# Performance work log

Hardware: AMD Instinct MI355X
Metric: run time of the kernel (lower is better)

The kernel has to match this reference:

```python
import jax, jax.numpy as jnp
import numpy as np


def setup_inputs() -> dict:
    key = jax.random.key(0)
    k_in, k_w = jax.random.split(key)
    input = jax.random.normal(k_in, (16, 64, 64, 512), dtype=jnp.float32)
    weight = jax.random.normal(k_w, (512, 512), dtype=jnp.float32)
    return {"input": input, "weight": weight}


def reference(input, weight):
    # Faithful to the torch source, including its quirky (weight*weight).sum(0)
    # (sum over the vocab axis -> (embed_dim,) vector, broadcast over vocab
    # columns; valid here because vocab_size == embed_dim).
    batch_dims, embed_dim = input.shape[:-1], input.shape[-1]
    x = input.reshape(-1, embed_dim)                     # (N, D)
    dists = -2.0 * jnp.einsum("nd,vd->nv", x, weight) + jnp.sum(weight * weight, axis=0)[None, :]
    idxes = jnp.argmin(dists, axis=1)                    # (N,)
    values = weight[idxes].reshape(*batch_dims, embed_dim)
    return values
```

## Files before the change

### kernel.cpp

```cpp
#include <hip/hip_runtime.h>


#define DIM   512
#define VOCAB 512
#define EPS_GAP 0.18f
#define RBATCH 8

typedef float f32x4 __attribute__((ext_vector_type(4)));
typedef _Float16 f16x8 __attribute__((ext_vector_type(8)));
typedef unsigned long long u64;

__device__ inline u64 packkey(float s, int v){
    unsigned u = __float_as_uint(s);
    u = (u & 0x80000000u) ? ~u : (u | 0x80000000u);
    return (((u64)u) << 32) | (unsigned)(~v);
}
__device__ inline float keyscore(u64 k){
    unsigned e = (unsigned)(k >> 32);
    return __uint_as_float((e & 0x80000000u) ? (e & 0x7fffffffu) : ~e);
}
__device__ inline int keyv(u64 k){ return (int)(~(unsigned)(k & 0xffffffffu)); }
__device__ inline u64 umax64(u64 a, u64 b){ return a > b ? a : b; }
__device__ inline u64 umin64(u64 a, u64 b){ return a < b ? a : b; }

__global__ void colsumsq_kernel(const float* __restrict__ w, float* __restrict__ c){
    const int v = blockIdx.x;
    const int lane = threadIdx.x;
    double s = 0.0;
    for (int i = lane; i < DIM; i += 64){
        const float wv = w[i * VOCAB + v];
        s += (double)wv * (double)wv;
    }
    #pragma unroll
    for (int m = 1; m <= 32; m <<= 1) s += __shfl_xor(s, m, 64);
    if (lane == 0) c[v] = (float)s;
}

__global__ void prep_w(const float* __restrict__ w,
                       _Float16* __restrict__ whc,
                       unsigned* __restrict__ cnt){
    const int i = blockIdx.x * 256 + threadIdx.x;
    const int v = i >> 9, k = i & 511;
    const int d = (k >> 5) * 16384 + ((k >> 3) & 3) * 4096 + v * 8 + (k & 7);
    whc[d] = (_Float16)w[i];
    if (i == 0) *cnt = 0u;
}

__launch_bounds__(256, 4)
__global__ void k1_scores(const float* __restrict__ x,
                          const _Float16* __restrict__ whc,
                          const float* __restrict__ cg,
                          const float* __restrict__ w,
                          float* __restrict__ out,
                          int* __restrict__ list,
                          unsigned* __restrict__ cnt){
    __shared__ __align__(16) _Float16 Ah[16384];
    __shared__ u64 mergeK[32][4][2];
    __shared__ int idx_s[32];

    const int t = threadIdx.x;
    const int lane = t & 63, wv = t >> 6, quad = lane >> 4, lm = lane & 15;
    const int cb = wv << 7;
    const long rbase = (long)blockIdx.x * 32;
    const float* xblk = x + rbase * DIM;

    f32x4 acc[2][8];
    #pragma unroll
    for (int ct = 0; ct < 8; ++ct){
        const float bias = -0.5f * cg[cb + ct * 16 + lm];
        f32x4 z; z[0] = bias; z[1] = bias; z[2] = bias; z[3] = bias;
        acc[0][ct] = z; acc[1][ct] = z;
    }

    #pragma unroll 4
    for (int jj = 0; jj < 16; ++jj){
        const int j   = jj * 256 + t;
        const int row = (j >> 3) & 31;
        const int k4  = (j & 7) | ((j >> 8) << 3);
        const int kk  = k4 << 2;
        const float4 a4 = *(const float4*)(xblk + (long)row * DIM + kk);
        union { _Float16 h[4]; ushort4 u; } cv;
        cv.h[0] = (_Float16)a4.x;
        cv.h[1] = (_Float16)a4.y;
        cv.h[2] = (_Float16)a4.z;
        cv.h[3] = (_Float16)a4.w;
        const int d = (((kk >> 5) * 4 + ((kk >> 3) & 3)) * 32 + row) * 8 + (kk & 7);
        *(ushort4*)&Ah[d] = cv.u;
    }
    __syncthreads();

    for (int ch = 0; ch < 16; ++ch){
        f16x8 ah0 = *(const f16x8*)&Ah[((ch * 4 + quad) * 32 + lm) * 8];
        f16x8 ah1 = *(const f16x8*)&Ah[((ch * 4 + quad) * 32 + 16 + lm) * 8];
        const _Float16* bb = whc + ch * 16384 + quad * 4096;
        #pragma unroll
        for (int ct = 0; ct < 8; ++ct){
            const f16x8 bh = *(const f16x8*)(bb + (cb + ct * 16 + lm) * 8);
            acc[0][ct] = __builtin_amdgcn_mfma_f32_16x16x32_f16(ah0, bh, acc[0][ct], 0, 0, 0);
            acc[1][ct] = __builtin_amdgcn_mfma_f32_16x16x32_f16(ah1, bh, acc[1][ct], 0, 0, 0);
        }
    }

    #pragma unroll
    for (int rt = 0; rt < 2; ++rt){
        #pragma unroll
        for (int reg = 0; reg < 4; ++reg){
            u64 b1 = 0, b2 = 0;
            #pragma unroll
            for (int ct = 0; ct < 8; ++ct){
                const u64 key = packkey(acc[rt][ct][reg], cb + ct * 16 + lm);
                if (key > b1){ b2 = b1; b1 = key; }
                else if (key > b2){ b2 = key; }
            }
            #pragma unroll
            for (int m = 1; m <= 8; m <<= 1){
                const u64 o1 = __shfl_xor(b1, m, 64);
                const u64 o2 = __shfl_xor(b2, m, 64);
                const u64 n1 = umax64(b1, o1);
                b2 = umax64(umin64(b1, o1), umax64(b2, o2));
                b1 = n1;
            }
            if (lm == 0){
                const int row = rt * 16 + quad * 4 + reg;
                mergeK[row][wv][0] = b1;
                mergeK[row][wv][1] = b2;
            }
        }
    }
    __syncthreads();
    if (t < 32){
        u64 p1 = mergeK[t][0][0], p2 = mergeK[t][0][1];
        #pragma unroll
        for (int i = 1; i < 4; ++i){
            const u64 q1 = mergeK[t][i][0], q2 = mergeK[t][i][1];
            const u64 n1 = umax64(p1, q1);
            p2 = umax64(umin64(p1, q1), umax64(p2, q2));
            p1 = n1;
        }
        idx_s[t] = keyv(p1);
        if (keyscore(p1) - keyscore(p2) < EPS_GAP){
            const unsigned p = atomicAdd(cnt, 1u);
            list[p] = (int)(rbase + t);
        }
    }
    __syncthreads();

    for (int rr = 0; rr < 32; rr += 2){
        const int row  = rr + (t >> 7);
        const int col  = (t & 127) << 2;
        const int vidx = idx_s[row];
        const float4 val = *(const float4*)(w + (long)vidx * DIM + col);
        *(float4*)(out + (rbase + row) * DIM + col) = val;
    }
}

__global__ void refine_rows(const float* __restrict__ x, const float* __restrict__ w,
                            const float* __restrict__ cg, const int* __restrict__ list,
                            const unsigned* __restrict__ cnt, float* __restrict__ out){
    __shared__ __align__(16) float xs[RBATCH][DIM];
    __shared__ u64 wk[RBATCH][4];
    __shared__ int bestv_s[RBATCH];
    const int t = threadIdx.x;
    const int lane = t & 63, wvq = t >> 6;
    const int n = (int)*cnt;
    for (int base = blockIdx.x * RBATCH; base < n; base += gridDim.x * RBATCH){
        const int m = (n - base < RBATCH) ? (n - base) : RBATCH;
        __syncthreads();
        for (int s = t; s < m * 128; s += 256){
            const int r = s >> 7, c = (s & 127) << 2;
            *(float4*)&xs[r][c] = *(const float4*)(x + (long)list[base + r] * DIM + c);
        }
        __syncthreads();
        u64 best[RBATCH];
        #pragma unroll
        for (int r = 0; r < RBATCH; ++r) best[r] = 0;
        #pragma unroll
        for (int vv = 0; vv < 2; ++vv){
            const int v = t + vv * 256;
            const float* wr = w + (long)v * DIM;
            float s[RBATCH];
            #pragma unroll
            for (int r = 0; r < RBATCH; ++r) s[r] = -0.5f * cg[v];
            for (int k = 0; k < DIM; k += 4){
                const float4 w4 = *(const float4*)(wr + k);
                #pragma unroll
                for (int r = 0; r < RBATCH; ++r){
                    const float4 x4 = *(const float4*)&xs[r][k];
                    s[r] = fmaf(w4.x, x4.x, s[r]);
                    s[r] = fmaf(w4.y, x4.y, s[r]);
                    s[r] = fmaf(w4.z, x4.z, s[r]);
                    s[r] = fmaf(w4.w, x4.w, s[r]);
                }
            }
            #pragma unroll
            for (int r = 0; r < RBATCH; ++r)
                best[r] = umax64(best[r], packkey(s[r], v));
        }
        #pragma unroll
        for (int r = 0; r < RBATCH; ++r){
            u64 b = best[r];
            #pragma unroll
            for (int mm = 1; mm <= 32; mm <<= 1) b = umax64(b, __shfl_xor(b, mm, 64));
            if (lane == 0) wk[r][wvq] = b;
        }
        __syncthreads();
        if (t < RBATCH){
            const u64 b = umax64(umax64(wk[t][0], wk[t][1]), umax64(wk[t][2], wk[t][3]));
            bestv_s[t] = keyv(b);
        }
        __syncthreads();
        for (int s = t; s < m * 128; s += 256){
            const int r = s >> 7, c = (s & 127) << 2;
            *(float4*)(out + (long)list[base + r] * DIM + c) =
                *(const float4*)(w + (long)bestv_s[r] * DIM + c);
        }
    }
}

__launch_bounds__(256)
__global__ void fallback_full(const float* __restrict__ x, const float* __restrict__ w,
                              float* __restrict__ out){
    __shared__ __align__(16) float As[16][68];
    __shared__ __align__(16) float Bs[16][VOCAB];
    __shared__ int   idx_sf[64];
    __shared__ float c_s[VOCAB];

    const int t  = threadIdx.x;
    const int tx = t & 31;
    const int ty = t >> 5;
    const long rbase = (long)blockIdx.x * 64;
    const float* xblk = x + rbase * DIM;

    for (int vv = t; vv < VOCAB; vv += 256){
        double s = 0.0;
        for (int i = 0; i < DIM; ++i){
            const float wvv = w[i * VOCAB + vv];
            s += (double)wvv * (double)wvv;
        }
        c_s[vv] = (float)s;
    }

    float acc[8][16];
    #pragma unroll
    for (int r = 0; r < 8; ++r)
        #pragma unroll
        for (int j = 0; j < 16; ++j) acc[r][j] = 0.0f;

    for (int k0 = 0; k0 < DIM; k0 += 16){
        __syncthreads();
        {
            const int r  = t >> 2;
            const int kq = (t & 3) << 2;
            const float4 a4 = *(const float4*)(xblk + (long)r * DIM + k0 + kq);
            As[kq + 0][r] = a4.x; As[kq + 1][r] = a4.y;
            As[kq + 2][r] = a4.z; As[kq + 3][r] = a4.w;
        }
        #pragma unroll
        for (int vb = 0; vb < 8; ++vb){
            const int v  = (t >> 2) + (vb << 6);
            const int kq = (t & 3) << 2;
            const float4 b4 = *(const float4*)(w + (long)v * DIM + k0 + kq);
            Bs[kq + 0][v] = b4.x; Bs[kq + 1][v] = b4.y;
            Bs[kq + 2][v] = b4.z; Bs[kq + 3][v] = b4.w;
        }
        __syncthreads();

        #pragma unroll
        for (int k = 0; k < 16; ++k){
            float a[8];
            const float4 a03 = *(const float4*)&As[k][ty * 8];
            const float4 a47 = *(const float4*)&As[k][ty * 8 + 4];
            a[0] = a03.x; a[1] = a03.y; a[2] = a03.z; a[3] = a03.w;
            a[4] = a47.x; a[5] = a47.y; a[6] = a47.z; a[7] = a47.w;
            float b[16];
            #pragma unroll
            for (int j = 0; j < 16; ++j) b[j] = Bs[k][tx + (j << 5)];
            #pragma unroll
            for (int r = 0; r < 8; ++r)
                #pragma unroll
                for (int j = 0; j < 16; ++j)
                    acc[r][j] = fmaf(a[r], b[j], acc[r][j]);
        }
    }

    #pragma unroll
    for (int r = 0; r < 8; ++r){
        float best = acc[r][0] - 0.5f * c_s[tx];
        int   bv   = tx;
        #pragma unroll
        for (int j = 1; j < 16; ++j){
            const float s = acc[r][j] - 0.5f * c_s[tx + (j << 5)];
            if (s > best){ best = s; bv = tx + (j << 5); }
        }
        unsigned u = __float_as_uint(best);
        u = (u & 0x80000000u) ? ~u : (u | 0x80000000u);
        u64 key = ((u64)u << 32) | (unsigned)(~(unsigned)bv);
        #pragma unroll
        for (int m = 1; m <= 16; m <<= 1){
            const u64 o = __shfl_xor(key, m, 64);
            if (o > key) key = o;
        }
        if (tx == 0) idx_sf[ty * 8 + r] = (int)(~(unsigned)(key & 0xFFFFFFFFull));
    }
    __syncthreads();

    for (int rr = 0; rr < 64; rr += 2){
        const int row  = rr + (t >> 7);
        const int col  = (t & 127) << 2;
        const int vidx = idx_sf[row];
        const float4 val = *(const float4*)(w + (long)vidx * DIM + col);
        *(float4*)(out + (rbase + row) * DIM + col) = val;
    }
}

extern "C" void kernel_launch(void* const* d_in, const int* in_sizes, int n_in,
                              void* d_out, int out_size, void* d_ws, size_t ws_size,
                              hipStream_t stream){
    const float* x = (const float*)d_in[0];
    const float* w = (const float*)d_in[1];
    float* out = (float*)d_out;
    const int rows = in_sizes[0] / DIM;

    const size_t whc_off  = 0;
    const size_t c_off    = whc_off + (size_t)DIM * VOCAB * 2;
    const size_t list_off = c_off   + (size_t)VOCAB * 4;
    const size_t cnt_off  = list_off + (size_t)rows * 4;
    const size_t need     = cnt_off + 16;

    if (ws_size >= need){
        _Float16* whc  = (_Float16*)((char*)d_ws + whc_off);
        float*    c    = (float*)((char*)d_ws + c_off);
        int*      list = (int*)((char*)d_ws + list_off);
        unsigned* cnt  = (unsigned*)((char*)d_ws + cnt_off);

        prep_w<<<(DIM * VOCAB) / 256, 256, 0, stream>>>(w, whc, cnt);
        colsumsq_kernel<<<VOCAB, 64, 0, stream>>>(w, c);
        k1_scores<<<rows / 32, 256, 0, stream>>>(x, whc, c, w, out, list, cnt);
        refine_rows<<<512, 256, 0, stream>>>(x, w, c, list, cnt, out);
    } else {
        fallback_full<<<rows / 64, 256, 0, stream>>>(x, w, out);
    }
}
```

Measured before the change: 331.0 us.

## Fuse weight prep with column norms and split gather into separate kernel

Replaces the separate fp16 weight-conversion and column-sum-of-squares kernels with one coalesced kernel that accumulates norms via double atomics into a memset-cleared buffer. Moves the output gather out of the scoring kernel into a dedicated kernel driven by a per-row index array in workspace. Also raises the unroll of the input-staging loop. This adds a memset and an extra launch plus index round-trip through global memory, but frees the scoring kernel from the gather tail and removes the strided column-sum reads.

```diff
diff --git a/kernel.cpp b/kernel.cpp
--- a/kernel.cpp
+++ b/kernel.cpp
@@ -23,40 +23,38 @@
 __device__ inline u64 umax64(u64 a, u64 b){ return a > b ? a : b; }
 __device__ inline u64 umin64(u64 a, u64 b){ return a < b ? a : b; }
 
-__global__ void colsumsq_kernel(const float* __restrict__ w, float* __restrict__ c){
-    const int v = blockIdx.x;
-    const int lane = threadIdx.x;
-    double s = 0.0;
-    for (int i = lane; i < DIM; i += 64){
-        const float wv = w[i * VOCAB + v];
-        s += (double)wv * (double)wv;
-    }
-    #pragma unroll
-    for (int m = 1; m <= 32; m <<= 1) s += __shfl_xor(s, m, 64);
-    if (lane == 0) c[v] = (float)s;
-}
-
-__global__ void prep_w(const float* __restrict__ w,
-                       _Float16* __restrict__ whc,
-                       unsigned* __restrict__ cnt){
-    const int i = blockIdx.x * 256 + threadIdx.x;
-    const int v = i >> 9, k = i & 511;
-    const int d = (k >> 5) * 16384 + ((k >> 3) & 3) * 4096 + v * 8 + (k & 7);
-    whc[d] = (_Float16)w[i];
-    if (i == 0) *cnt = 0u;
+__global__ void prep_fused(const float* __restrict__ w,
+                           _Float16* __restrict__ whc,
+                           double* __restrict__ cgd){
+    const int t  = threadIdx.x;
+    const int r0 = blockIdx.x * 4;
+    const int c0 = t * 2;
+    double s0 = 0.0, s1 = 0.0;
+    #pragma unroll
+    for (int rr = 0; rr < 4; ++rr){
+        const int row = r0 + rr;
+        const float2 v = *(const float2*)(w + (long)row * VOCAB + c0);
+        s0 += (double)v.x * (double)v.x;
+        s1 += (double)v.y * (double)v.y;
+        union { _Float16 h[2]; unsigned u; } cv;
+        cv.h[0] = (_Float16)v.x;
+        cv.h[1] = (_Float16)v.y;
+        const int d = ((c0 >> 5) * 16384) + (((c0 >> 3) & 3) * 4096) + row * 8 + (c0 & 7);
+        *(unsigned*)&whc[d] = cv.u;
+    }
+    atomicAdd(&cgd[c0],     s0);
+    atomicAdd(&cgd[c0 + 1], s1);
 }
 
 __launch_bounds__(256, 4)
 __global__ void k1_scores(const float* __restrict__ x,
                           const _Float16* __restrict__ whc,
-                          const float* __restrict__ cg,
-                          const float* __restrict__ w,
-                          float* __restrict__ out,
+                          const double* __restrict__ cgd,
+                          int* __restrict__ idx,
                           int* __restrict__ list,
                           unsigned* __restrict__ cnt){
     __shared__ __align__(16) _Float16 Ah[16384];
     __shared__ u64 mergeK[32][4][2];
-    __shared__ int idx_s[32];
 
     const int t = threadIdx.x;
     const int lane = t & 63, wv = t >> 6, quad = lane >> 4, lm = lane & 15;
@@ -67,12 +65,12 @@
     f32x4 acc[2][8];
     #pragma unroll
     for (int ct = 0; ct < 8; ++ct){
-        const float bias = -0.5f * cg[cb + ct * 16 + lm];
+        const float bias = -0.5f * (float)cgd[cb + ct * 16 + lm];
         f32x4 z; z[0] = bias; z[1] = bias; z[2] = bias; z[3] = bias;
         acc[0][ct] = z; acc[1][ct] = z;
     }
 
-    #pragma unroll 4
+    #pragma unroll 8
     for (int jj = 0; jj < 16; ++jj){
         const int j   = jj * 256 + t;
         const int row = (j >> 3) & 31;
@@ -137,25 +135,31 @@
             p2 = umax64(umin64(p1, q1), umax64(p2, q2));
             p1 = n1;
         }
-        idx_s[t] = keyv(p1);
+        idx[rbase + t] = keyv(p1);
         if (keyscore(p1) - keyscore(p2) < EPS_GAP){
             const unsigned p = atomicAdd(cnt, 1u);
             list[p] = (int)(rbase + t);
         }
     }
-    __syncthreads();
-
-    for (int rr = 0; rr < 32; rr += 2){
-        const int row  = rr + (t >> 7);
-        const int col  = (t & 127) << 2;
-        const int vidx = idx_s[row];
-        const float4 val = *(const float4*)(w + (long)vidx * DIM + col);
-        *(float4*)(out + (rbase + row) * DIM + col) = val;
+}
+
+__global__ void gather_rows(const float* __restrict__ w,
+                            const int* __restrict__ idx,
+                            float* __restrict__ out){
+    const int t = threadIdx.x;
+    #pragma unroll 4
+    for (int g = 0; g < 16; ++g){
+        const long flat = ((long)blockIdx.x * 16 + g) * 256 + t;
+        const int  row  = (int)(flat >> 7);
+        const int  c4   = (int)(flat & 127);
+        const int  vidx = idx[row];
+        const float4 val = *(const float4*)(w + (long)vidx * DIM + c4 * 4);
+        *(float4*)(out + flat * 4) = val;
     }
 }
 
 __global__ void refine_rows(const float* __restrict__ x, const float* __restrict__ w,
-                            const float* __restrict__ cg, const int* __restrict__ list,
+                            const double* __restrict__ cgd, const int* __restrict__ list,
                             const unsigned* __restrict__ cnt, float* __restrict__ out){
     __shared__ __align__(16) float xs[RBATCH][DIM];
     __shared__ u64 wk[RBATCH][4];
@@ -180,7 +184,7 @@
             const float* wr = w + (long)v * DIM;
             float s[RBATCH];
             #pragma unroll
-            for (int r = 0; r < RBATCH; ++r) s[r] = -0.5f * cg[v];
+            for (int r = 0; r < RBATCH; ++r) s[r] = -0.5f * (float)cgd[v];
             for (int k = 0; k < DIM; k += 4){
                 const float4 w4 = *(const float4*)(wr + k);
                 #pragma unroll
@@ -322,21 +326,24 @@
     const int rows = in_sizes[0] / DIM;
 
     const size_t whc_off  = 0;
-    const size_t c_off    = whc_off + (size_t)DIM * VOCAB * 2;
-    const size_t list_off = c_off   + (size_t)VOCAB * 4;
-    const size_t cnt_off  = list_off + (size_t)rows * 4;
-    const size_t need     = cnt_off + 16;
+    const size_t cgd_off  = whc_off + (size_t)DIM * VOCAB * 2;
+    const size_t cnt_off  = cgd_off + (size_t)VOCAB * 8;
+    const size_t idx_off  = cnt_off + 64;
+    const size_t list_off = idx_off + (size_t)rows * 4;
+    const size_t need     = list_off + (size_t)rows * 4;
 
     if (ws_size >= need){
         _Float16* whc  = (_Float16*)((char*)d_ws + whc_off);
-        float*    c    = (float*)((char*)d_ws + c_off);
+        double*   cgd  = (double*)((char*)d_ws + cgd_off);
+        unsigned* cnt  = (unsigned*)((char*)d_ws + cnt_off);
+        int*      idx  = (int*)((char*)d_ws + idx_off);
         int*      list = (int*)((char*)d_ws + list_off);
-        unsigned* cnt  = (unsigned*)((char*)d_ws + cnt_off);
-
-        prep_w<<<(DIM * VOCAB) / 256, 256, 0, stream>>>(w, whc, cnt);
-        colsumsq_kernel<<<VOCAB, 64, 0, stream>>>(w, c);
-        k1_scores<<<rows / 32, 256, 0, stream>>>(x, whc, c, w, out, list, cnt);
-        refine_rows<<<512, 256, 0, stream>>>(x, w, c, list, cnt, out);
+
+        hipMemsetAsync((char*)d_ws + cgd_off, 0, (size_t)VOCAB * 8 + 64, stream);
+        prep_fused<<<VOCAB / 4, 256, 0, stream>>>(w, whc, cgd);
+        k1_scores<<<rows / 32, 256, 0, stream>>>(x, whc, cgd, idx, list, cnt);
+        gather_rows<<<rows / 32, 256, 0, stream>>>(w, idx, out);
+        refine_rows<<<512, 256, 0, stream>>>(x, w, cgd, list, cnt, out);
     } else {
         fallback_full<<<rows / 64, 256, 0, stream>>>(x, w, out);
     }
```

After: 342.0 us. 3.3% more time.
